# Optimization experiments

Hardware: AMD Instinct MI355X
Metric: run time of the kernel (lower is better)

The kernel has to match this reference:

```python
import jax, jax.numpy as jnp
import numpy as np

B, C, H, W = 4, 256, 64, 64
CH = C // 2  # inner channels


def setup_inputs() -> dict:
    key = jax.random.key(0)
    ks = jax.random.split(key, 9)
    s_in = 1.0 / np.sqrt(C)
    s_w = 1.0 / np.sqrt(CH)
    return {
        "x": jax.random.normal(ks[0], (B, C, H, W), dtype=jnp.float32),
        "theta_w": jax.random.normal(ks[1], (CH, C), dtype=jnp.float32) * s_in,
        "theta_b": jax.random.normal(ks[2], (CH,), dtype=jnp.float32) * s_in,
        "phi_w": jax.random.normal(ks[3], (CH, C), dtype=jnp.float32) * s_in,
        "phi_b": jax.random.normal(ks[4], (CH,), dtype=jnp.float32) * s_in,
        "g_w": jax.random.normal(ks[5], (CH, C), dtype=jnp.float32) * s_in,
        "g_b": jax.random.normal(ks[6], (CH,), dtype=jnp.float32) * s_in,
        "W_w": jax.random.normal(ks[7], (C, CH), dtype=jnp.float32) * s_w,
        "W_b": jax.random.normal(ks[8], (C,), dtype=jnp.float32) * s_w,
    }


def _proj(x_flat, w, b):
    # 1x1 conv == channel matmul; x_flat: [B, C, N] -> [B, O, N]
    return jnp.einsum("oc,bcn->bon", w, x_flat) + b[None, :, None]


def reference(x, theta_w, theta_b, phi_w, phi_b, g_w, g_b, W_w, W_b):
    b, c, h, w = x.shape
    n = h * w
    xf = x.reshape(b, c, n)
    theta = _proj(xf, theta_w, theta_b)  # [B, CH, N]
    phi = _proj(xf, phi_w, phi_b)        # [B, CH, N]
    g = _proj(xf, g_w, g_b)              # [B, CH, N]
    # scores[b,i,j] = theta[:, :, i] . phi[:, :, j]; softmax over j
    attn = jax.nn.softmax(jnp.einsum("bci,bcj->bij", theta, phi), axis=-1)
    # torch: bmm(g_x, attn) -> out[b,c,i] = sum_j g[b,c,j] * attn[b,j,i]
    out = jnp.einsum("bcj,bji->bci", g, attn)  # [B, CH, N]
    out = jnp.einsum("oc,bcn->bon", W_w, out) + W_b[None, :, None]
    return out.reshape(b, c, h, w) + x
```

## Files before the change

### kernel.cpp

```cpp
#include <hip/hip_runtime.h>
#include <math.h>

#define BB    4
#define CC    256
#define CHN   128
#define NN    4096
#define NHALF 2048

typedef short short8 __attribute__((ext_vector_type(8)));
typedef float f32x4  __attribute__((ext_vector_type(4)));
typedef unsigned short u16;
typedef u16  us4 __attribute__((ext_vector_type(4)));

#define MFMA16(a, b, c) __builtin_amdgcn_mfma_f32_16x16x32_bf16((a), (b), (c), 0, 0, 0)

static __device__ __forceinline__ u16 f2bf(float f) {
    union { float f; unsigned u; } v; v.f = f;
    unsigned r = v.u + 0x7FFFu + ((v.u >> 16) & 1u);
    return (u16)(r >> 16);
}
static __device__ __forceinline__ float bf2f(u16 h) {
    union { unsigned u; float f; } v; v.u = ((unsigned)h) << 16;
    return v.f;
}
static __device__ __forceinline__ int sw128(int row, int u) {
    return row * 128 + ((u ^ (row & 7)) << 3);
}

__global__ __launch_bounds__(256) void k_cvtw(
    const float* __restrict__ tw, const float* __restrict__ pw,
    const float* __restrict__ gw, u16* __restrict__ wbf)
{
    int idx = (blockIdx.x * 256 + threadIdx.x) * 4;
    const float* s = (idx < 32768) ? tw : (idx < 65536 ? pw : gw);
    float4 v = *(const float4*)(s + (idx & 32767));
    us4 r = { f2bf(v.x), f2bf(v.y), f2bf(v.z), f2bf(v.w) };
    *(us4*)(wbf + idx) = r;
}

__global__ __launch_bounds__(256) void k_proj(
    const float* __restrict__ x, const u16* __restrict__ wbf,
    const float* __restrict__ tb, const float* __restrict__ pb,
    const float* __restrict__ gbias,
    u16* __restrict__ tht, u16* __restrict__ pht, u16* __restrict__ gg)
{
    __shared__ u16 xs[64 * 264];
    __shared__ u16 ws[128 * 264];
    const int tid = threadIdx.x;
    const int n0  = blockIdx.x * 64;
    const int b   = blockIdx.y;
    const int w   = tid >> 6;
    const int ln  = tid & 15;
    const int q   = (tid >> 4) & 3;
    const int mq  = w >> 1, nq = w & 1;

    for (int p = 0; p < 16; ++p) {
        int c   = p * 16 + (tid >> 4);
        int nl4 = (tid & 15) * 4;
        float4 xv = *(const float4*)(x + ((size_t)b * CC + c) * NN + n0 + nl4);
        xs[(nl4 + 0) * 264 + c] = f2bf(xv.x);
        xs[(nl4 + 1) * 264 + c] = f2bf(xv.y);
        xs[(nl4 + 2) * 264 + c] = f2bf(xv.z);
        xs[(nl4 + 3) * 264 + c] = f2bf(xv.w);
    }

    for (int pr = 0; pr < 3; ++pr) {
        __syncthreads();
        const u16* wsrc = wbf + pr * (CHN * CC);
        for (int p = 0; p < 16; ++p) {
            int idx = p * 256 + tid;
            int row = idx >> 5, u = idx & 31;
            short8 v = *(const short8*)(wsrc + row * 256 + u * 8);
            *(short8*)(&ws[row * 264 + u * 8]) = v;
        }
        __syncthreads();

        f32x4 acc[4][2];
        for (int mt = 0; mt < 4; ++mt)
            for (int nt = 0; nt < 2; ++nt) acc[mt][nt] = (f32x4){0.f, 0.f, 0.f, 0.f};

        for (int ks = 0; ks < 8; ++ks) {
            int u = ks * 4 + q;
            short8 a[4], bx[2];
            #pragma unroll
            for (int mt = 0; mt < 4; ++mt)
                a[mt] = *(const short8*)(&ws[(mq*64 + mt*16 + ln) * 264 + u * 8]);
            #pragma unroll
            for (int nt = 0; nt < 2; ++nt)
                bx[nt] = *(const short8*)(&xs[(nq*32 + nt*16 + ln) * 264 + u * 8]);
            #pragma unroll
            for (int mt = 0; mt < 4; ++mt)
                #pragma unroll
                for (int nt = 0; nt < 2; ++nt)
                    acc[mt][nt] = MFMA16(a[mt], bx[nt], acc[mt][nt]);
        }

        const float* bias = (pr == 0) ? tb : (pr == 1 ? pb : gbias);
        if (pr < 2) {
            u16* dst = (pr == 0) ? tht : pht;
            for (int mt = 0; mt < 4; ++mt) {
                int ob = mq*64 + mt*16 + q*4;
                float4 bv = *(const float4*)(bias + ob);
                for (int nt = 0; nt < 2; ++nt) {
                    int n = n0 + nq*32 + nt*16 + ln;
                    f32x4 v = acc[mt][nt];
                    us4 r = { f2bf(v.x + bv.x), f2bf(v.y + bv.y),
                              f2bf(v.z + bv.z), f2bf(v.w + bv.w) };
                    *(us4*)(dst + ((size_t)b * NN + n) * CHN + ob) = r;
                }
            }
        } else {
            __syncthreads();
            u16* gbuf = ws;
            for (int mt = 0; mt < 4; ++mt) {
                int ob = mq*64 + mt*16 + q*4;
                float4 bv = *(const float4*)(bias + ob);
                for (int nt = 0; nt < 2; ++nt) {
                    int nl = nq*32 + nt*16 + ln;
                    f32x4 v = acc[mt][nt];
                    gbuf[(ob + 0) * 68 + nl] = f2bf(v.x + bv.x);
                    gbuf[(ob + 1) * 68 + nl] = f2bf(v.y + bv.y);
                    gbuf[(ob + 2) * 68 + nl] = f2bf(v.z + bv.z);
                    gbuf[(ob + 3) * 68 + nl] = f2bf(v.w + bv.w);
                }
            }
            __syncthreads();
            for (int p = 0; p < 8; ++p) {
                int idx = p * 256 + tid;
                int c = idx >> 4, n4 = (idx & 15) * 4;
                us4 r = *(const us4*)(&gbuf[c * 68 + n4]);
                *(us4*)(gg + ((size_t)b * CHN + c) * NN + n0 + n4) = r;
            }
        }
    }
}

__global__ __launch_bounds__(256) void k_rowsum(
    const u16* __restrict__ tht, const u16* __restrict__ pht,
    float* __restrict__ Z)
{
    __shared__ u16 th_s[64 * 128];
    __shared__ u16 ph_s[256 * 128];
    __shared__ float zs[64][4];
    const int tid = threadIdx.x;
    const int j0  = blockIdx.x * 64;
    const int b   = blockIdx.y;
    const int w   = tid >> 6;
    const int ln  = tid & 15;
    const int q   = (tid >> 4) & 3;

    {
        const u16* src = tht + ((size_t)b * NN + j0) * CHN;
        for (int p = 0; p < 4; ++p) {
            int idx = p * 256 + tid;
            int row = idx >> 4, u = idx & 15;
            short8 v = *(const short8*)(src + row * 128 + u * 8);
            *(short8*)(&th_s[sw128(row, u)]) = v;
        }
    }

    float zp[4][4];
    for (int jt = 0; jt < 4; ++jt)
        for (int r = 0; r < 4; ++r) zp[jt][r] = 0.f;

    for (int is = 0; is < 16; ++is) {
        __syncthreads();
        const u16* src = pht + ((size_t)b * NN + is * 256) * CHN;
        for (int p = 0; p < 16; ++p) {
            int idx = p * 256 + tid;
            int row = idx >> 4, u = idx & 15;
            short8 v = *(const short8*)(src + row * 128 + u * 8);
            *(short8*)(&ph_s[sw128(row, u)]) = v;
        }
        __syncthreads();

        f32x4 s[4][4];
        for (int jt = 0; jt < 4; ++jt)
            for (int it = 0; it < 4; ++it) s[jt][it] = (f32x4){0.f, 0.f, 0.f, 0.f};
        for (int ks = 0; ks < 4; ++ks) {
            int u = ks * 4 + q;
            short8 a[4], bfr[4];
            #pragma unroll
            for (int jt = 0; jt < 4; ++jt)
                a[jt] = *(const short8*)(&th_s[sw128(jt*16 + ln, u)]);
            #pragma unroll
            for (int it = 0; it < 4; ++it)
                bfr[it] = *(const short8*)(&ph_s[sw128(w*64 + it*16 + ln, u)]);
            #pragma unroll
            for (int jt = 0; jt < 4; ++jt)
                #pragma unroll
                for (int it = 0; it < 4; ++it)
                    s[jt][it] = MFMA16(a[jt], bfr[it], s[jt][it]);
        }
        for (int jt = 0; jt < 4; ++jt)
            for (int it = 0; it < 4; ++it) {
                f32x4 v = s[jt][it];
                zp[jt][0] += __expf(v.x);
                zp[jt][1] += __expf(v.y);
                zp[jt][2] += __expf(v.z);
                zp[jt][3] += __expf(v.w);
            }
    }

    for (int jt = 0; jt < 4; ++jt)
        for (int r = 0; r < 4; ++r) {
            float v = zp[jt][r];
            v += __shfl_xor(v, 1);
            v += __shfl_xor(v, 2);
            v += __shfl_xor(v, 4);
            v += __shfl_xor(v, 8);
            if (ln == 0) zs[jt*16 + q*4 + r][w] = v;
        }
    __syncthreads();
    if (tid < 64)
        Z[(size_t)b * NN + j0 + tid] = zs[tid][0] + zs[tid][1] + zs[tid][2] + zs[tid][3];
}

__global__ __launch_bounds__(256) void k_fold(
    const u16* __restrict__ gg, const float* __restrict__ Z,
    u16* __restrict__ gp)
{
    const int b = blockIdx.y;
    int base = (blockIdx.x * 256 + threadIdx.x) * 8;
    int n = base & (NN - 1);
    int c = base >> 12;
    size_t off = ((size_t)b * CHN + c) * NN + n;
    short8 gv = *(const short8*)(gg + off);
    const float* zp = Z + (size_t)b * NN + n;
    short8 r;
    #pragma unroll
    for (int k = 0; k < 8; ++k) {
        float f = bf2f(((u16*)&gv)[k]) / zp[k];
        ((u16*)&r)[k] = f2bf(f);
    }
    *(short8*)(gp + off) = r;
}

__global__ __launch_bounds__(256) void k_attn(
    const u16* __restrict__ tht, const u16* __restrict__ pht,
    const u16* __restrict__ gp, float* __restrict__ inner)
{
    __shared__ u16 ph_s[128 * 128];
    __shared__ u16 th_s[128 * 128];
    __shared__ u16 gp_s[128 * 128];
    __shared__ u16 E_s [128 * 128];
    const int tid  = threadIdx.x;
    const int i0   = blockIdx.x * 128;
    const int half = blockIdx.y;
    const int b    = blockIdx.z;
    const int w    = tid >> 6;
    const int ln   = tid & 15;
    const int q    = (tid >> 4) & 3;
    const int wq1  = w >> 1, wq0 = w & 1;

    {
        const u16* src = pht + ((size_t)b * NN + i0) * CHN;
        for (int p = 0; p < 8; ++p) {
            int idx = p * 256 + tid;
            int row = idx >> 4, u = idx & 15;
            short8 v = *(const short8*)(src + row * 128 + u * 8);
            *(short8*)(&ph_s[sw128(row, u)]) = v;
        }
    }

    f32x4 pacc[4][4];
    for (int ii = 0; ii < 4; ++ii)
        for (int cc = 0; cc < 4; ++cc) pacc[ii][cc] = (f32x4){0.f, 0.f, 0.f, 0.f};

    for (int js = 0; js < 16; ++js) {
        const int j0 = half * NHALF + js * 128;
        __syncthreads();
        {
            const u16* src = tht + ((size_t)b * NN + j0) * CHN;
            for (int p = 0; p < 8; ++p) {
                int idx = p * 256 + tid;
                int row = idx >> 4, u = idx & 15;
                short8 v = *(const short8*)(src + row * 128 + u * 8);
                *(short8*)(&th_s[sw128(row, u)]) = v;
            }
        }
        {
            const u16* src = gp + (size_t)b * CHN * NN + j0;
            for (int p = 0; p < 8; ++p) {
                int idx = p * 256 + tid;
                int row = idx >> 4, u = idx & 15;
                short8 v = *(const short8*)(src + (size_t)row * NN + u * 8);
                *(short8*)(&gp_s[sw128(row, u)]) = v;
            }
        }
        __syncthreads();

        f32x4 s[4][4];
        for (int jj = 0; jj < 4; ++jj)
            for (int ii = 0; ii < 4; ++ii) s[jj][ii] = (f32x4){0.f, 0.f, 0.f, 0.f};
        for (int ks = 0; ks < 4; ++ks) {
            int u = ks * 4 + q;
            short8 a[4], bf[4];
            #pragma unroll
            for (int jj = 0; jj < 4; ++jj)
                a[jj] = *(const short8*)(&th_s[sw128(wq1*64 + jj*16 + ln, u)]);
            #pragma unroll
            for (int ii = 0; ii < 4; ++ii)
                bf[ii] = *(const short8*)(&ph_s[sw128(wq0*64 + ii*16 + ln, u)]);
            #pragma unroll
            for (int jj = 0; jj < 4; ++jj)
                #pragma unroll
                for (int ii = 0; ii < 4; ++ii)
                    s[jj][ii] = MFMA16(a[jj], bf[ii], s[jj][ii]);
        }
        for (int jj = 0; jj < 4; ++jj) {
            int jl  = wq1*64 + jj*16 + q*4;
            int u   = jl >> 3, off = jl & 7;
            for (int ii = 0; ii < 4; ++ii) {
                int ri = wq0*64 + ii*16 + ln;
                f32x4 v = s[jj][ii];
                us4 e = { f2bf(__expf(v.x)), f2bf(__expf(v.y)),
                          f2bf(__expf(v.z)), f2bf(__expf(v.w)) };
                *(us4*)(&E_s[ri*128 + ((u ^ (ri & 7)) << 3) + off]) = e;
            }
        }
        __syncthreads();

        for (int ks = 0; ks < 4; ++ks) {
            int u = ks * 4 + q;
            short8 ae[4], bg[4];
            #pragma unroll
            for (int ii = 0; ii < 4; ++ii)
                ae[ii] = *(const short8*)(&E_s[sw128(wq1*64 + ii*16 + ln, u)]);
            #pragma unroll
            for (int cc = 0; cc < 4; ++cc)
                bg[cc] = *(const short8*)(&gp_s[sw128(wq0*64 + cc*16 + ln, u)]);
            #pragma unroll
            for (int ii = 0; ii < 4; ++ii)
                #pragma unroll
                for (int cc = 0; cc < 4; ++cc)
                    pacc[ii][cc] = MFMA16(ae[ii], bg[cc], pacc[ii][cc]);
        }
    }

    float* dst = inner + ((size_t)half * BB + b) * CHN * (size_t)NN;
    for (int ii = 0; ii < 4; ++ii) {
        int i = i0 + wq1*64 + ii*16 + q*4;
        for (int cc = 0; cc < 4; ++cc) {
            int c = wq0*64 + cc*16 + ln;
            *(f32x4*)(dst + (size_t)c * NN + i) = pacc[ii][cc];
        }
    }
}

__global__ __launch_bounds__(256) void k_final(
    const float* __restrict__ inner, const float* __restrict__ x,
    const float* __restrict__ Ww, const float* __restrict__ Wb,
    float* __restrict__ out)
{
    const int n  = blockIdx.x * 256 + threadIdx.x;
    const int o0 = blockIdx.y * 16;
    const int b  = blockIdx.z;
    const float* i0p = inner + (size_t)b * CHN * NN + n;
    const float* i1p = i0p + (size_t)BB * CHN * NN;

    float acc[16];
    #pragma unroll
    for (int k = 0; k < 16; ++k) acc[k] = Wb[o0 + k];
    #pragma unroll 4
    for (int c = 0; c < CHN; ++c) {
        float iv = i0p[(size_t)c * NN] + i1p[(size_t)c * NN];
        #pragma unroll
        for (int k = 0; k < 16; ++k)
            acc[k] += Ww[(o0 + k) * CHN + c] * iv;
    }
    #pragma unroll
    for (int k = 0; k < 16; ++k) {
        size_t idx = ((size_t)b * CC + o0 + k) * NN + n;
        out[idx] = acc[k] + x[idx];
    }
}

extern "C" void kernel_launch(void* const* d_in, const int* in_sizes, int n_in,
                              void* d_out, int out_size, void* d_ws, size_t ws_size,
                              hipStream_t stream)
{
    const float* x  = (const float*)d_in[0];
    const float* tw = (const float*)d_in[1];
    const float* tb = (const float*)d_in[2];
    const float* pw = (const float*)d_in[3];
    const float* pb = (const float*)d_in[4];
    const float* gw = (const float*)d_in[5];
    const float* gb = (const float*)d_in[6];
    const float* Ww = (const float*)d_in[7];
    const float* Wb = (const float*)d_in[8];
    float* out = (float*)d_out;

    char* p = (char*)d_ws;
    const size_t proj_u16 = (size_t)BB * NN * CHN;
    u16*   tht   = (u16*)p;            p += proj_u16 * 2;
    u16*   pht   = (u16*)p;            p += proj_u16 * 2;
    u16*   gg    = (u16*)p;            p += proj_u16 * 2;
    u16*   gp    = (u16*)p;            p += proj_u16 * 2;
    u16*   wbf   = (u16*)p;            p += (size_t)3 * CHN * CC * 2;
    float* Z     = (float*)p;          p += (size_t)BB * NN * 4;
    float* inner = (float*)p;

    k_cvtw  <<<96, 256, 0, stream>>>(tw, pw, gw, wbf);
    k_proj  <<<dim3(NN / 64, BB), 256, 0, stream>>>(x, wbf, tb, pb, gb, tht, pht, gg);
    k_rowsum<<<dim3(NN / 64, BB), 256, 0, stream>>>(tht, pht, Z);
    k_fold  <<<dim3(CHN * NN / 2048, BB), 256, 0, stream>>>(gg, Z, gp);
    k_attn  <<<dim3(NN / 128, 2, BB), 256, 0, stream>>>(tht, pht, gp, inner);
    k_final <<<dim3(NN / 256, CC / 16, BB), 256, 0, stream>>>(inner, x, Ww, Wb, out);
}
```

Baseline: 229.6 us.

## Restructure non-local attention pipeline: fold normalization into log-sum, MFMA final projection

Removes the separate fold kernel by storing log row-sums and initializing score accumulators with the negated log, so the exponent already includes the normalization. The attention kernel moves to 512-thread blocks with 256-row tiles, a four-way split over j, direct global loads of theta and g fragments instead of LDS staging, and bf16 transposed partial outputs. The final 1x1 conv becomes an MFMA kernel using bf16 W weights converted in k_cvtw, replacing the scalar FP32 loop. The projection and rowsum kernels also switch to 512 threads with register-held fragments. The risks are extra bf16 rounding of the intermediate and final-projection inputs, and uncoalesced global fragment loads.

```diff
diff --git a/kernel.cpp b/kernel.cpp
--- a/kernel.cpp
+++ b/kernel.cpp
@@ -5,7 +5,6 @@
 #define CC    256
 #define CHN   128
 #define NN    4096
-#define NHALF 2048
 
 typedef short short8 __attribute__((ext_vector_type(8)));
 typedef float f32x4  __attribute__((ext_vector_type(4)));
@@ -19,115 +18,97 @@
     unsigned r = v.u + 0x7FFFu + ((v.u >> 16) & 1u);
     return (u16)(r >> 16);
 }
-static __device__ __forceinline__ float bf2f(u16 h) {
-    union { unsigned u; float f; } v; v.u = ((unsigned)h) << 16;
-    return v.f;
-}
 static __device__ __forceinline__ int sw128(int row, int u) {
     return row * 128 + ((u ^ (row & 7)) << 3);
 }
 
 __global__ __launch_bounds__(256) void k_cvtw(
     const float* __restrict__ tw, const float* __restrict__ pw,
-    const float* __restrict__ gw, u16* __restrict__ wbf)
+    const float* __restrict__ gw, const float* __restrict__ Ww,
+    u16* __restrict__ wall)
 {
     int idx = (blockIdx.x * 256 + threadIdx.x) * 4;
-    const float* s = (idx < 32768) ? tw : (idx < 65536 ? pw : gw);
+    const float* s = (idx < 32768) ? tw
+                   : (idx < 65536) ? pw
+                   : (idx < 98304) ? gw : Ww;
     float4 v = *(const float4*)(s + (idx & 32767));
     us4 r = { f2bf(v.x), f2bf(v.y), f2bf(v.z), f2bf(v.w) };
-    *(us4*)(wbf + idx) = r;
-}
-
-__global__ __launch_bounds__(256) void k_proj(
-    const float* __restrict__ x, const u16* __restrict__ wbf,
+    *(us4*)(wall + idx) = r;
+}
+
+__global__ __launch_bounds__(512) void k_proj(
+    const float* __restrict__ x, const u16* __restrict__ wall,
     const float* __restrict__ tb, const float* __restrict__ pb,
     const float* __restrict__ gbias,
     u16* __restrict__ tht, u16* __restrict__ pht, u16* __restrict__ gg)
 {
     __shared__ u16 xs[64 * 264];
-    __shared__ u16 ws[128 * 264];
+    __shared__ u16 gbuf[128 * 68];
     const int tid = threadIdx.x;
     const int n0  = blockIdx.x * 64;
     const int b   = blockIdx.y;
-    const int w   = tid >> 6;
-    const int ln  = tid & 15;
-    const int q   = (tid >> 4) & 3;
-    const int mq  = w >> 1, nq = w & 1;
-
-    for (int p = 0; p < 16; ++p) {
-        int c   = p * 16 + (tid >> 4);
-        int nl4 = (tid & 15) * 4;
-        float4 xv = *(const float4*)(x + ((size_t)b * CC + c) * NN + n0 + nl4);
-        xs[(nl4 + 0) * 264 + c] = f2bf(xv.x);
-        xs[(nl4 + 1) * 264 + c] = f2bf(xv.y);
-        xs[(nl4 + 2) * 264 + c] = f2bf(xv.z);
-        xs[(nl4 + 3) * 264 + c] = f2bf(xv.w);
-    }
+    const int ln  = tid & 15, q = (tid >> 4) & 3, wid = tid >> 6;
+    const int ow  = wid & 1, nw = wid >> 1;
+
+    for (int p = 0; p < 8; ++p) {
+        int id = p * 512 + tid;
+        int c = id >> 4, n4 = (id & 15) * 4;
+        float4 xv = *(const float4*)(x + ((size_t)b * CC + c) * NN + n0 + n4);
+        xs[(n4 + 0) * 264 + c] = f2bf(xv.x);
+        xs[(n4 + 1) * 264 + c] = f2bf(xv.y);
+        xs[(n4 + 2) * 264 + c] = f2bf(xv.z);
+        xs[(n4 + 3) * 264 + c] = f2bf(xv.w);
+    }
+    __syncthreads();
+
+    short8 bfr[8];
+    #pragma unroll
+    for (int ks = 0; ks < 8; ++ks)
+        bfr[ks] = *(const short8*)(&xs[(nw * 16 + ln) * 264 + ks * 32 + q * 8]);
 
     for (int pr = 0; pr < 3; ++pr) {
-        __syncthreads();
-        const u16* wsrc = wbf + pr * (CHN * CC);
-        for (int p = 0; p < 16; ++p) {
-            int idx = p * 256 + tid;
-            int row = idx >> 5, u = idx & 31;
-            short8 v = *(const short8*)(wsrc + row * 256 + u * 8);
-            *(short8*)(&ws[row * 264 + u * 8]) = v;
-        }
-        __syncthreads();
-
-        f32x4 acc[4][2];
-        for (int mt = 0; mt < 4; ++mt)
-            for (int nt = 0; nt < 2; ++nt) acc[mt][nt] = (f32x4){0.f, 0.f, 0.f, 0.f};
-
+        const u16* wsrc = wall + pr * 32768;
+        f32x4 acc[4];
+        #pragma unroll
+        for (int oo = 0; oo < 4; ++oo) acc[oo] = (f32x4){0.f, 0.f, 0.f, 0.f};
         for (int ks = 0; ks < 8; ++ks) {
-            int u = ks * 4 + q;
-            short8 a[4], bx[2];
-            #pragma unroll
-            for (int mt = 0; mt < 4; ++mt)
-                a[mt] = *(const short8*)(&ws[(mq*64 + mt*16 + ln) * 264 + u * 8]);
-            #pragma unroll
-            for (int nt = 0; nt < 2; ++nt)
-                bx[nt] = *(const short8*)(&xs[(nq*32 + nt*16 + ln) * 264 + u * 8]);
-            #pragma unroll
-            for (int mt = 0; mt < 4; ++mt)
-                #pragma unroll
-                for (int nt = 0; nt < 2; ++nt)
-                    acc[mt][nt] = MFMA16(a[mt], bx[nt], acc[mt][nt]);
-        }
-
+            short8 a[4];
+            #pragma unroll
+            for (int oo = 0; oo < 4; ++oo)
+                a[oo] = *(const short8*)(wsrc + (size_t)(ow*64 + oo*16 + ln) * 256 + ks*32 + q*8);
+            #pragma unroll
+            for (int oo = 0; oo < 4; ++oo)
+                acc[oo] = MFMA16(a[oo], bfr[ks], acc[oo]);
+        }
         const float* bias = (pr == 0) ? tb : (pr == 1 ? pb : gbias);
         if (pr < 2) {
             u16* dst = (pr == 0) ? tht : pht;
-            for (int mt = 0; mt < 4; ++mt) {
-                int ob = mq*64 + mt*16 + q*4;
-                float4 bv = *(const float4*)(bias + ob);
-                for (int nt = 0; nt < 2; ++nt) {
-                    int n = n0 + nq*32 + nt*16 + ln;
-                    f32x4 v = acc[mt][nt];
-                    us4 r = { f2bf(v.x + bv.x), f2bf(v.y + bv.y),
-                              f2bf(v.z + bv.z), f2bf(v.w + bv.w) };
-                    *(us4*)(dst + ((size_t)b * NN + n) * CHN + ob) = r;
-                }
+            const int n = n0 + nw * 16 + ln;
+            #pragma unroll
+            for (int oo = 0; oo < 4; ++oo) {
+                int o = ow * 64 + oo * 16 + q * 4;
+                float4 bv = *(const float4*)(bias + o);
+                f32x4 v = acc[oo];
+                us4 r = { f2bf(v.x + bv.x), f2bf(v.y + bv.y),
+                          f2bf(v.z + bv.z), f2bf(v.w + bv.w) };
+                *(us4*)(dst + ((size_t)b * NN + n) * CHN + o) = r;
             }
         } else {
+            const int nl = nw * 16 + ln;
+            #pragma unroll
+            for (int oo = 0; oo < 4; ++oo) {
+                int o = ow * 64 + oo * 16 + q * 4;
+                float4 bv = *(const float4*)(bias + o);
+                f32x4 v = acc[oo];
+                gbuf[(o + 0) * 68 + nl] = f2bf(v.x + bv.x);
+                gbuf[(o + 1) * 68 + nl] = f2bf(v.y + bv.y);
+                gbuf[(o + 2) * 68 + nl] = f2bf(v.z + bv.z);
+                gbuf[(o + 3) * 68 + nl] = f2bf(v.w + bv.w);
+            }
             __syncthreads();
-            u16* gbuf = ws;
-            for (int mt = 0; mt < 4; ++mt) {
-                int ob = mq*64 + mt*16 + q*4;
-                float4 bv = *(const float4*)(bias + ob);
-                for (int nt = 0; nt < 2; ++nt) {
-                    int nl = nq*32 + nt*16 + ln;
-                    f32x4 v = acc[mt][nt];
-                    gbuf[(ob + 0) * 68 + nl] = f2bf(v.x + bv.x);
-                    gbuf[(ob + 1) * 68 + nl] = f2bf(v.y + bv.y);
-                    gbuf[(ob + 2) * 68 + nl] = f2bf(v.z + bv.z);
-                    gbuf[(ob + 3) * 68 + nl] = f2bf(v.w + bv.w);
-                }
-            }
-            __syncthreads();
-            for (int p = 0; p < 8; ++p) {
-                int idx = p * 256 + tid;
-                int c = idx >> 4, n4 = (idx & 15) * 4;
+            for (int p = 0; p < 4; ++p) {
+                int id = p * 512 + tid;
+                int c = id >> 4, n4 = (id & 15) * 4;
                 us4 r = *(const us4*)(&gbuf[c * 68 + n4]);
                 *(us4*)(gg + ((size_t)b * CHN + c) * NN + n0 + n4) = r;
             }
@@ -135,184 +116,152 @@
     }
 }
 
-__global__ __launch_bounds__(256) void k_rowsum(
+__global__ __launch_bounds__(512) void k_rowsum(
     const u16* __restrict__ tht, const u16* __restrict__ pht,
-    float* __restrict__ Z)
-{
-    __shared__ u16 th_s[64 * 128];
+    float* __restrict__ Lbuf)
+{
     __shared__ u16 ph_s[256 * 128];
     __shared__ float zs[64][4];
     const int tid = threadIdx.x;
     const int j0  = blockIdx.x * 64;
     const int b   = blockIdx.y;
-    const int w   = tid >> 6;
-    const int ln  = tid & 15;
-    const int q   = (tid >> 4) & 3;
-
-    {
-        const u16* src = tht + ((size_t)b * NN + j0) * CHN;
-        for (int p = 0; p < 4; ++p) {
-            int idx = p * 256 + tid;
-            int row = idx >> 4, u = idx & 15;
-            short8 v = *(const short8*)(src + row * 128 + u * 8);
-            *(short8*)(&th_s[sw128(row, u)]) = v;
-        }
-    }
-
-    float zp[4][4];
-    for (int jt = 0; jt < 4; ++jt)
-        for (int r = 0; r < 4; ++r) zp[jt][r] = 0.f;
+    const int ln  = tid & 15, q = (tid >> 4) & 3, wid = tid >> 6;
+    const int jw  = wid & 1, iw = wid >> 1;
+    const u16* thb = tht + (size_t)b * NN * CHN;
+    const u16* phb = pht + (size_t)b * NN * CHN;
+
+    float zp[2][4];
+    #pragma unroll
+    for (int jj = 0; jj < 2; ++jj)
+        #pragma unroll
+        for (int r = 0; r < 4; ++r) zp[jj][r] = 0.f;
 
     for (int is = 0; is < 16; ++is) {
+        for (int p = 0; p < 8; ++p) {
+            int id = p * 512 + tid;
+            int row = id >> 4, u = id & 15;
+            short8 v = *(const short8*)(phb + (size_t)(is * 256 + row) * 128 + u * 8);
+            *(short8*)(&ph_s[sw128(row, u)]) = v;
+        }
         __syncthreads();
-        const u16* src = pht + ((size_t)b * NN + is * 256) * CHN;
-        for (int p = 0; p < 16; ++p) {
-            int idx = p * 256 + tid;
-            int row = idx >> 4, u = idx & 15;
-            short8 v = *(const short8*)(src + row * 128 + u * 8);
-            *(short8*)(&ph_s[sw128(row, u)]) = v;
-        }
+
+        f32x4 s[2][4];
+        #pragma unroll
+        for (int jj = 0; jj < 2; ++jj)
+            #pragma unroll
+            for (int ii = 0; ii < 4; ++ii) s[jj][ii] = (f32x4){0.f, 0.f, 0.f, 0.f};
+        for (int ks = 0; ks < 4; ++ks) {
+            short8 a[2], bb[4];
+            #pragma unroll
+            for (int jj = 0; jj < 2; ++jj)
+                a[jj] = *(const short8*)(thb + (size_t)(j0 + jw*32 + jj*16 + ln) * 128 + ks*32 + q*8);
+            #pragma unroll
+            for (int ii = 0; ii < 4; ++ii)
+                bb[ii] = *(const short8*)(&ph_s[sw128(iw*64 + ii*16 + ln, ks*4 + q)]);
+            #pragma unroll
+            for (int jj = 0; jj < 2; ++jj)
+                #pragma unroll
+                for (int ii = 0; ii < 4; ++ii)
+                    s[jj][ii] = MFMA16(a[jj], bb[ii], s[jj][ii]);
+        }
+        #pragma unroll
+        for (int jj = 0; jj < 2; ++jj)
+            #pragma unroll
+            for (int ii = 0; ii < 4; ++ii) {
+                f32x4 v = s[jj][ii];
+                zp[jj][0] += __expf(v.x);
+                zp[jj][1] += __expf(v.y);
+                zp[jj][2] += __expf(v.z);
+                zp[jj][3] += __expf(v.w);
+            }
         __syncthreads();
-
-        f32x4 s[4][4];
-        for (int jt = 0; jt < 4; ++jt)
-            for (int it = 0; it < 4; ++it) s[jt][it] = (f32x4){0.f, 0.f, 0.f, 0.f};
-        for (int ks = 0; ks < 4; ++ks) {
-            int u = ks * 4 + q;
-            short8 a[4], bfr[4];
-            #pragma unroll
-            for (int jt = 0; jt < 4; ++jt)
-                a[jt] = *(const short8*)(&th_s[sw128(jt*16 + ln, u)]);
-            #pragma unroll
-            for (int it = 0; it < 4; ++it)
-                bfr[it] = *(const short8*)(&ph_s[sw128(w*64 + it*16 + ln, u)]);
-            #pragma unroll
-            for (int jt = 0; jt < 4; ++jt)
-                #pragma unroll
-                for (int it = 0; it < 4; ++it)
-                    s[jt][it] = MFMA16(a[jt], bfr[it], s[jt][it]);
-        }
-        for (int jt = 0; jt < 4; ++jt)
-            for (int it = 0; it < 4; ++it) {
-                f32x4 v = s[jt][it];
-                zp[jt][0] += __expf(v.x);
-                zp[jt][1] += __expf(v.y);
-                zp[jt][2] += __expf(v.z);
-                zp[jt][3] += __expf(v.w);
-            }
-    }
-
-    for (int jt = 0; jt < 4; ++jt)
+    }
+
+    #pragma unroll
+    for (int jj = 0; jj < 2; ++jj)
+        #pragma unroll
         for (int r = 0; r < 4; ++r) {
-            float v = zp[jt][r];
+            float v = zp[jj][r];
             v += __shfl_xor(v, 1);
             v += __shfl_xor(v, 2);
             v += __shfl_xor(v, 4);
             v += __shfl_xor(v, 8);
-            if (ln == 0) zs[jt*16 + q*4 + r][w] = v;
+            if (ln == 0) zs[jw*32 + jj*16 + q*4 + r][iw] = v;
         }
     __syncthreads();
     if (tid < 64)
-        Z[(size_t)b * NN + j0 + tid] = zs[tid][0] + zs[tid][1] + zs[tid][2] + zs[tid][3];
-}
-
-__global__ __launch_bounds__(256) void k_fold(
-    const u16* __restrict__ gg, const float* __restrict__ Z,
-    u16* __restrict__ gp)
-{
-    const int b = blockIdx.y;
-    int base = (blockIdx.x * 256 + threadIdx.x) * 8;
-    int n = base & (NN - 1);
-    int c = base >> 12;
-    size_t off = ((size_t)b * CHN + c) * NN + n;
-    short8 gv = *(const short8*)(gg + off);
-    const float* zp = Z + (size_t)b * NN + n;
-    short8 r;
-    #pragma unroll
-    for (int k = 0; k < 8; ++k) {
-        float f = bf2f(((u16*)&gv)[k]) / zp[k];
-        ((u16*)&r)[k] = f2bf(f);
-    }
-    *(short8*)(gp + off) = r;
-}
-
-__global__ __launch_bounds__(256) void k_attn(
+        Lbuf[(size_t)b * NN + j0 + tid] =
+            __logf(zs[tid][0] + zs[tid][1] + zs[tid][2] + zs[tid][3]);
+}
+
+__global__ __launch_bounds__(512, 2) void k_attn(
     const u16* __restrict__ tht, const u16* __restrict__ pht,
-    const u16* __restrict__ gp, float* __restrict__ inner)
-{
-    __shared__ u16 ph_s[128 * 128];
-    __shared__ u16 th_s[128 * 128];
-    __shared__ u16 gp_s[128 * 128];
-    __shared__ u16 E_s [128 * 128];
-    const int tid  = threadIdx.x;
-    const int i0   = blockIdx.x * 128;
-    const int half = blockIdx.y;
-    const int b    = blockIdx.z;
-    const int w    = tid >> 6;
-    const int ln   = tid & 15;
-    const int q    = (tid >> 4) & 3;
-    const int wq1  = w >> 1, wq0 = w & 1;
+    const u16* __restrict__ gg, const float* __restrict__ Lbuf,
+    u16* __restrict__ innerT)
+{
+    __shared__ u16 ph_s[256 * 128];
+    __shared__ u16 E_s [256 * 128];
+    const int tid = threadIdx.x;
+    const int i0  = blockIdx.x * 256;
+    const int jq  = blockIdx.y;
+    const int b   = blockIdx.z;
+    const int ln  = tid & 15, q = (tid >> 4) & 3, wid = tid >> 6;
+    const int g1  = wid & 1;
+    const int g2  = wid >> 1;
+
+    const u16*  thb = tht + (size_t)b * NN * CHN;
+    const u16*  ggb = gg  + (size_t)b * CHN * NN;
+    const float* Lb = Lbuf + (size_t)b * NN;
 
     {
         const u16* src = pht + ((size_t)b * NN + i0) * CHN;
         for (int p = 0; p < 8; ++p) {
-            int idx = p * 256 + tid;
-            int row = idx >> 4, u = idx & 15;
+            int id = p * 512 + tid;
+            int row = id >> 4, u = id & 15;
             short8 v = *(const short8*)(src + row * 128 + u * 8);
             *(short8*)(&ph_s[sw128(row, u)]) = v;
         }
     }
 
     f32x4 pacc[4][4];
-    for (int ii = 0; ii < 4; ++ii)
-        for (int cc = 0; cc < 4; ++cc) pacc[ii][cc] = (f32x4){0.f, 0.f, 0.f, 0.f};
-
-    for (int js = 0; js < 16; ++js) {
-        const int j0 = half * NHALF + js * 128;
+    #pragma unroll
+    for (int cc = 0; cc < 4; ++cc)
+        #pragma unroll
+        for (int ii = 0; ii < 4; ++ii) pacc[cc][ii] = (f32x4){0.f, 0.f, 0.f, 0.f};
+
+    for (int js = 0; js < 8; ++js) {
+        const int j0 = jq * 1024 + js * 128;
         __syncthreads();
-        {
-            const u16* src = tht + ((size_t)b * NN + j0) * CHN;
-            for (int p = 0; p < 8; ++p) {
-                int idx = p * 256 + tid;
-                int row = idx >> 4, u = idx & 15;
-                short8 v = *(const short8*)(src + row * 128 + u * 8);
-                *(short8*)(&th_s[sw128(row, u)]) = v;
-            }
-        }
-        {
-            const u16* src = gp + (size_t)b * CHN * NN + j0;
-            for (int p = 0; p < 8; ++p) {
-                int idx = p * 256 + tid;
-                int row = idx >> 4, u = idx & 15;
-                short8 v = *(const short8*)(src + (size_t)row * NN + u * 8);
-                *(short8*)(&gp_s[sw128(row, u)]) = v;
-            }
-        }
-        __syncthreads();
 
         f32x4 s[4][4];
-        for (int jj = 0; jj < 4; ++jj)
-            for (int ii = 0; ii < 4; ++ii) s[jj][ii] = (f32x4){0.f, 0.f, 0.f, 0.f};
+        #pragma unroll
+        for (int jj = 0; jj < 4; ++jj) {
+            float4 Lv = *(const float4*)(Lb + j0 + g1*64 + jj*16 + q*4);
+            f32x4 init = { -Lv.x, -Lv.y, -Lv.z, -Lv.w };
+            #pragma unroll
+            for (int ii = 0; ii < 4; ++ii) s[jj][ii] = init;
+        }
         for (int ks = 0; ks < 4; ++ks) {
-            int u = ks * 4 + q;
-            short8 a[4], bf[4];
+            short8 a[4], bb[4];
             #pragma unroll
             for (int jj = 0; jj < 4; ++jj)
-                a[jj] = *(const short8*)(&th_s[sw128(wq1*64 + jj*16 + ln, u)]);
+                a[jj] = *(const short8*)(thb + (size_t)(j0 + g1*64 + jj*16 + ln) * 128 + ks*32 + q*8);
             #pragma unroll
             for (int ii = 0; ii < 4; ++ii)
-                bf[ii] = *(const short8*)(&ph_s[sw128(wq0*64 + ii*16 + ln, u)]);
+                bb[ii] = *(const short8*)(&ph_s[sw128(g2*64 + ii*16 + ln, ks*4 + q)]);
             #pragma unroll
             for (int jj = 0; jj < 4; ++jj)
                 #pragma unroll
                 for (int ii = 0; ii < 4; ++ii)
-                    s[jj][ii] = MFMA16(a[jj], bf[ii], s[jj][ii]);
-        }
+                    s[jj][ii] = MFMA16(a[jj], bb[ii], s[jj][ii]);
+        }
+        #pragma unroll
         for (int jj = 0; jj < 4; ++jj) {
-            int jl  = wq1*64 + jj*16 + q*4;
-            int u   = jl >> 3, off = jl & 7;
+            int jl = g1*64 + jj*16 + q*4;
+            int u = jl >> 3, off = jl & 7;
+            #pragma unroll
             for (int ii = 0; ii < 4; ++ii) {
-                int ri = wq0*64 + ii*16 + ln;
+                int ri = g2*64 + ii*16 + ln;
                 f32x4 v = s[jj][ii];
                 us4 e = { f2bf(__expf(v.x)), f2bf(__expf(v.y)),
                           f2bf(__expf(v.z)), f2bf(__expf(v.w)) };
@@ -322,58 +271,81 @@
         __syncthreads();
 
         for (int ks = 0; ks < 4; ++ks) {
-            int u = ks * 4 + q;
-            short8 ae[4], bg[4];
+            short8 a[4], bb[4];
+            #pragma unroll
+            for (int cc = 0; cc < 4; ++cc)
+                a[cc] = *(const short8*)(ggb + (size_t)(g1*64 + cc*16 + ln) * NN + j0 + ks*32 + q*8);
             #pragma unroll
             for (int ii = 0; ii < 4; ++ii)
-                ae[ii] = *(const short8*)(&E_s[sw128(wq1*64 + ii*16 + ln, u)]);
+                bb[ii] = *(const short8*)(&E_s[sw128(g2*64 + ii*16 + ln, ks*4 + q)]);
             #pragma unroll
             for (int cc = 0; cc < 4; ++cc)
-                bg[cc] = *(const short8*)(&gp_s[sw128(wq0*64 + cc*16 + ln, u)]);
-            #pragma unroll
-            for (int ii = 0; ii < 4; ++ii)
                 #pragma unroll
-                for (int cc = 0; cc < 4; ++cc)
-                    pacc[ii][cc] = MFMA16(ae[ii], bg[cc], pacc[ii][cc]);
-        }
-    }
-
-    float* dst = inner + ((size_t)half * BB + b) * CHN * (size_t)NN;
-    for (int ii = 0; ii < 4; ++ii) {
-        int i = i0 + wq1*64 + ii*16 + q*4;
-        for (int cc = 0; cc < 4; ++cc) {
-            int c = wq0*64 + cc*16 + ln;
-            *(f32x4*)(dst + (size_t)c * NN + i) = pacc[ii][cc];
-        }
-    }
-}
-
-__global__ __launch_bounds__(256) void k_final(
-    const float* __restrict__ inner, const float* __restrict__ x,
-    const float* __restrict__ Ww, const float* __restrict__ Wb,
+                for (int ii = 0; ii < 4; ++ii)
+                    pacc[cc][ii] = MFMA16(a[cc], bb[ii], pacc[cc][ii]);
+        }
+    }
+
+    u16* dst = innerT + ((size_t)jq * BB + b) * (size_t)NN * CHN;
+    #pragma unroll
+    for (int cc = 0; cc < 4; ++cc)
+        #pragma unroll
+        for (int ii = 0; ii < 4; ++ii) {
+            int i = i0 + g2*64 + ii*16 + ln;
+            int c = g1*64 + cc*16 + q*4;
+            f32x4 v = pacc[cc][ii];
+            us4 r = { f2bf(v.x), f2bf(v.y), f2bf(v.z), f2bf(v.w) };
+            *(us4*)(dst + (size_t)i * CHN + c) = r;
+        }
+}
+
+__global__ __launch_bounds__(512) void k_final(
+    const u16* __restrict__ innerT, const float* __restrict__ x,
+    const u16* __restrict__ Wwbf, const float* __restrict__ Wb,
     float* __restrict__ out)
 {
-    const int n  = blockIdx.x * 256 + threadIdx.x;
-    const int o0 = blockIdx.y * 16;
-    const int b  = blockIdx.z;
-    const float* i0p = inner + (size_t)b * CHN * NN + n;
-    const float* i1p = i0p + (size_t)BB * CHN * NN;
-
-    float acc[16];
-    #pragma unroll
-    for (int k = 0; k < 16; ++k) acc[k] = Wb[o0 + k];
-    #pragma unroll 4
-    for (int c = 0; c < CHN; ++c) {
-        float iv = i0p[(size_t)c * NN] + i1p[(size_t)c * NN];
-        #pragma unroll
-        for (int k = 0; k < 16; ++k)
-            acc[k] += Ww[(o0 + k) * CHN + c] * iv;
-    }
-    #pragma unroll
-    for (int k = 0; k < 16; ++k) {
-        size_t idx = ((size_t)b * CC + o0 + k) * NN + n;
-        out[idx] = acc[k] + x[idx];
-    }
+    const int tid = threadIdx.x;
+    const int n0  = blockIdx.x * 64;
+    const int b   = blockIdx.y;
+    const int ln  = tid & 15, q = (tid >> 4) & 3, wid = tid >> 6;
+
+    f32x4 acc[4][2];
+    #pragma unroll
+    for (int nn = 0; nn < 4; ++nn)
+        #pragma unroll
+        for (int oo = 0; oo < 2; ++oo) acc[nn][oo] = (f32x4){0.f, 0.f, 0.f, 0.f};
+
+    for (int jq = 0; jq < 4; ++jq) {
+        const u16* src = innerT + ((size_t)jq * BB + b) * (size_t)NN * CHN;
+        for (int ks = 0; ks < 4; ++ks) {
+            short8 a[4], bw[2];
+            #pragma unroll
+            for (int nn = 0; nn < 4; ++nn)
+                a[nn] = *(const short8*)(src + (size_t)(n0 + nn*16 + ln) * CHN + ks*32 + q*8);
+            #pragma unroll
+            for (int oo = 0; oo < 2; ++oo)
+                bw[oo] = *(const short8*)(Wwbf + (size_t)(wid*32 + oo*16 + ln) * CHN + ks*32 + q*8);
+            #pragma unroll
+            for (int nn = 0; nn < 4; ++nn)
+                #pragma unroll
+                for (int oo = 0; oo < 2; ++oo)
+                    acc[nn][oo] = MFMA16(a[nn], bw[oo], acc[nn][oo]);
+        }
+    }
+    #pragma unroll
+    for (int nn = 0; nn < 4; ++nn)
+        #pragma unroll
+        for (int oo = 0; oo < 2; ++oo) {
+            int o = wid*32 + oo*16 + ln;
+            int n = n0 + nn*16 + q*4;
+            size_t idx = ((size_t)b * CC + o) * NN + n;
+            float4 xv = *(const float4*)(x + idx);
+            float wb = Wb[o];
+            f32x4 v = acc[nn][oo];
+            f32x4 r = { v.x + wb + xv.x, v.y + wb + xv.y,
+                        v.z + wb + xv.z, v.w + wb + xv.w };
+            *(f32x4*)(out + idx) = r;
+        }
 }
 
 extern "C" void kernel_launch(void* const* d_in, const int* in_sizes, int n_in,
@@ -393,18 +365,16 @@
 
     char* p = (char*)d_ws;
     const size_t proj_u16 = (size_t)BB * NN * CHN;
-    u16*   tht   = (u16*)p;            p += proj_u16 * 2;
-    u16*   pht   = (u16*)p;            p += proj_u16 * 2;
-    u16*   gg    = (u16*)p;            p += proj_u16 * 2;
-    u16*   gp    = (u16*)p;            p += proj_u16 * 2;
-    u16*   wbf   = (u16*)p;            p += (size_t)3 * CHN * CC * 2;
-    float* Z     = (float*)p;          p += (size_t)BB * NN * 4;
-    float* inner = (float*)p;
-
-    k_cvtw  <<<96, 256, 0, stream>>>(tw, pw, gw, wbf);
-    k_proj  <<<dim3(NN / 64, BB), 256, 0, stream>>>(x, wbf, tb, pb, gb, tht, pht, gg);
-    k_rowsum<<<dim3(NN / 64, BB), 256, 0, stream>>>(tht, pht, Z);
-    k_fold  <<<dim3(CHN * NN / 2048, BB), 256, 0, stream>>>(gg, Z, gp);
-    k_attn  <<<dim3(NN / 128, 2, BB), 256, 0, stream>>>(tht, pht, gp, inner);
-    k_final <<<dim3(NN / 256, CC / 16, BB), 256, 0, stream>>>(inner, x, Ww, Wb, out);
-}
+    u16*   tht    = (u16*)p;   p += proj_u16 * 2;
+    u16*   pht    = (u16*)p;   p += proj_u16 * 2;
+    u16*   gg     = (u16*)p;   p += proj_u16 * 2;
+    u16*   wall   = (u16*)p;   p += (size_t)131072 * 2;
+    float* Lbuf   = (float*)p; p += (size_t)BB * NN * 4;
+    u16*   innerT = (u16*)p;
+
+    k_cvtw  <<<128, 256, 0, stream>>>(tw, pw, gw, Ww, wall);
+    k_proj  <<<dim3(64, BB), 512, 0, stream>>>(x, wall, tb, pb, gb, tht, pht, gg);
+    k_rowsum<<<dim3(64, BB), 512, 0, stream>>>(tht, pht, Lbuf);
+    k_attn  <<<dim3(16, 4, BB), 512, 0, stream>>>(tht, pht, gg, Lbuf, innerT);
+    k_final <<<dim3(64, BB), 512, 0, stream>>>(innerT, x, wall + 98304, Wb, out);
+}
```

Result: slower. 242.7 us (+5.7%).
